# Performance work log

Hardware: AMD Instinct MI355X
Metric: run time of the kernel (lower is better)

Reference implementation:

```python
import jax, jax.numpy as jnp
import numpy as np

LN_EPS = 1e-5


def _layernorm(x, w, b):
    m = jnp.mean(x, axis=-1, keepdims=True)
    v = jnp.mean(jnp.square(x - m), axis=-1, keepdims=True)
    return (x - m) * jax.lax.rsqrt(v + LN_EPS) * w + b


def setup_inputs() -> dict:
    key = jax.random.key(0)
    k1, k2 = jax.random.split(key)
    B, S, D = 64, 512, 1024
    inputo = jax.random.normal(k1, (B, S, D), dtype=jnp.float32)
    W = jax.random.normal(k2, (2 * D, 4 * D), dtype=jnp.float32) * 0.02
    b = jnp.zeros((4 * D,), dtype=jnp.float32)
    ln_w = jnp.ones((4 * D,), dtype=jnp.float32)
    ln_b = jnp.zeros((4 * D,), dtype=jnp.float32)
    init_hx = jnp.zeros((1, D), dtype=jnp.float32)
    init_cx = jnp.zeros((1, D), dtype=jnp.float32)
    return {"inputo": inputo, "W": W, "b": b, "ln_w": ln_w, "ln_b": ln_b,
            "init_hx": init_hx, "init_cx": init_cx}


def reference(inputo, W, b, ln_w, ln_b, init_hx, init_cx):
    B, S, D = inputo.shape
    osize = init_hx.shape[1]
    hx = jnp.broadcast_to(init_hx, (B, osize))
    cx = jnp.broadcast_to(init_cx, (B, osize))

    def step(carry, x_t):
        h, c = carry
        comb = _layernorm(jnp.concatenate([x_t, h], axis=-1) @ W + b, ln_w, ln_b)
        comb = comb.reshape(B, 4, osize)
        gates = jax.nn.sigmoid(comb[:, :3])          # ig, fg, og
        hidden = jnp.tanh(comb[:, 3])
        c = gates[:, 1] * c + gates[:, 0] * hidden
        h = gates[:, 2] * jnp.tanh(c)
        return (h, c), h

    xs = jnp.swapaxes(inputo, 0, 1)                  # [S, B, D]
    _, outs = jax.lax.scan(step, (hx, cx), xs)       # [S, B, osize]
    return jnp.swapaxes(outs, 0, 1)                  # [B, S, osize]
```

## Files before the change

### kernel.cpp

```cpp
#include <hip/hip_runtime.h>
#include <hip/hip_bf16.h>


typedef __attribute__((ext_vector_type(8))) short bf16x8;
typedef __attribute__((ext_vector_type(16))) float f32x16;
typedef __attribute__((ext_vector_type(4)))  int   i32x4;

#define AT_RLX __ATOMIC_RELAXED
#define SC_AGT __HIP_MEMORY_SCOPE_AGENT


__global__ __launch_bounds__(256) void conv_w(const float* __restrict__ W,
                                              __hip_bfloat16* __restrict__ Wt) {
    size_t id = (size_t)blockIdx.x * 256 + threadIdx.x;
    int k = (int)(id >> 12);
    int n = (int)(id & 4095);
    Wt[(size_t)n * 2048 + k] = __float2bfloat16(W[id]);
}

__global__ __launch_bounds__(256) void conv_x(const float* __restrict__ X,
                                              __hip_bfloat16* __restrict__ Xt) {
    size_t id = (size_t)blockIdx.x * 256 + threadIdx.x;
    int d   = (int)(id & 1023);
    int row = (int)(id >> 10);
    int s = row >> 6;
    int b = row & 63;
    Xt[id] = __float2bfloat16(X[(((size_t)b * 512 + s) << 10) + d]);
}

__global__ __launch_bounds__(256) void init_misc(const float* __restrict__ hx,
                                                 __hip_bfloat16* __restrict__ h,
                                                 unsigned long long* __restrict__ comb2,
                                                 unsigned int* __restrict__ hflag) {
    int id = blockIdx.x * 256 + threadIdx.x;
    comb2[id] = 0ULL;
    if (id < 65536) h[id] = __float2bfloat16(hx[id & 1023]);
    if (id < 1024)  hflag[id] = 0u;
}

__device__ __forceinline__ i32x4 ld_cp16(const void* p) {
    i32x4 r;
    asm volatile("global_load_dwordx4 %0, %1, off sc0 sc1"
                 : "=&v"(r) : "v"(p) : "memory");
    return r;
}
__device__ __forceinline__ void vm_wait0() {
    asm volatile("s_waitcnt vmcnt(0)" ::: "memory");
    __builtin_amdgcn_sched_barrier(0);
}
__device__ __forceinline__ void xchg8u(unsigned long long* p, unsigned long long v) {
    unsigned long long old = __hip_atomic_exchange(p, v, AT_RLX, SC_AGT);
    asm volatile("" :: "v"(old));
}

__global__ __launch_bounds__(256, 1) void lstm_fused(
    const __hip_bfloat16* __restrict__ Xt,
    const __hip_bfloat16* __restrict__ Wt,
    __hip_bfloat16* __restrict__ h,
    const float* __restrict__ bias,
    const float* __restrict__ lnw,
    const float* __restrict__ lnb,
    const float* __restrict__ cx,
    unsigned long long* __restrict__ comb2,
    float* __restrict__ out,
    unsigned int* __restrict__ hflag)
{
    const int tid  = threadIdx.x;
    const int lane = tid & 63;
    const int wv   = tid >> 6;
    const int b    = blockIdx.x;

    const int nt = b >> 1;
    const int mt = b & 1;
    const int kc = wv;
    const int cl = lane & 31;
    const int hi = lane >> 5;
    const int kh = hi * 8;
    const int n0 = nt * 32;

    __shared__ float lds_f[8192];
    __shared__ short hstage[2][16384];
    __shared__ float red[8];

    const short* bp = (const short*)Wt + (size_t)(n0 + cl) * 2048 + kc * 512 + kh;
    bf16x8 breg[32];
#pragma unroll
    for (int i = 0; i < 32; ++i) breg[i] = *(const bf16x8*)(bp + i * 16);

    const short* xbase = (const short*)Xt + (size_t)(mt * 32 + cl) * 1024 + kc * 512 + kh;
    const short* hsrc = (const short*)h + (size_t)(mt * 32) * 1024 + (kc - 2) * 512 + lane * 8;
    const unsigned int* myhf = &hflag[(mt * 32 + cl) * 16];

    float cr[4];
    float bias_r[4][4], lnw_r[4][4], lnb_r[4][4];
    if (b < 64) {
#pragma unroll
        for (int e = 0; e < 4; ++e) cr[e] = cx[4 * tid + e];
#pragma unroll
        for (int g = 0; g < 4; ++g)
#pragma unroll
            for (int e = 0; e < 4; ++e) {
                bias_r[g][e] = bias[1024 * g + 4 * tid + e];
                lnw_r[g][e]  = lnw[1024 * g + 4 * tid + e];
                lnb_r[g][e]  = lnb[1024 * g + 4 * tid + e];
            }
    }

    for (int s = 0; s < 512; ++s) {
        f32x16 accA, accB;
#pragma unroll
        for (int i = 0; i < 16; ++i) { accA[i] = 0.f; accB[i] = 0.f; }
        if (kc < 2) {
            const short* ap = xbase + (size_t)s * 65536;
#pragma unroll
            for (int i = 0; i < 16; ++i) {
                bf16x8 a0 = *(const bf16x8*)(ap + i * 16);
                bf16x8 a1 = *(const bf16x8*)(ap + (i + 16) * 16);
                accA = __builtin_amdgcn_mfma_f32_32x32x16_bf16(a0, breg[i],      accA, 0, 0, 0);
                accB = __builtin_amdgcn_mfma_f32_32x32x16_bf16(a1, breg[i + 16], accB, 0, 0, 0);
            }
        } else {
            while (__hip_atomic_load(myhf, AT_RLX, SC_AGT) < (unsigned int)s)
                __builtin_amdgcn_s_sleep(1);
            asm volatile("" ::: "memory");
            i32x4 hb[32];
#pragma unroll
            for (int j = 0; j < 32; ++j)
                hb[j] = ld_cp16(hsrc + (size_t)j * 1024);
            vm_wait0();
            short* st = &hstage[kc - 2][0];
#pragma unroll
            for (int j = 0; j < 32; ++j)
                *(i32x4*)((char*)(st + j * 512) + ((lane * 16) ^ ((j & 7) << 4))) = hb[j];
            const char* rb = (const char*)(st + cl * 512);
            const int swz = (cl & 7) << 4;
#pragma unroll
            for (int i = 0; i < 16; ++i) {
                bf16x8 a0 = *(const bf16x8*)(rb + ((i * 32 + hi * 16) ^ swz));
                bf16x8 a1 = *(const bf16x8*)(rb + ((512 + i * 32 + hi * 16) ^ swz));
                accA = __builtin_amdgcn_mfma_f32_32x32x16_bf16(a0, breg[i],      accA, 0, 0, 0);
                accB = __builtin_amdgcn_mfma_f32_32x32x16_bf16(a1, breg[i + 16], accB, 0, 0, 0);
            }
        }
        float* lbuf = lds_f + (s & 1) * 4096;
#pragma unroll
        for (int r = 0; r < 16; ++r) {
            int rl = (r & 3) + 8 * (r >> 2) + 4 * (lane >> 5);
            lbuf[kc * 1024 + rl * 32 + cl] = accA[r] + accB[r];
        }
        __syncthreads();
        {
            unsigned long long ep64 = ((unsigned long long)(unsigned)(s + 1)) << 32;
#pragma unroll
            for (int half = 0; half < 2; ++half) {
                int e = 2 * tid + half * 512;
                float2 p0 = *(const float2*)&lbuf[e];
                float2 p1 = *(const float2*)&lbuf[1024 + e];
                float2 p2 = *(const float2*)&lbuf[2048 + e];
                float2 p3 = *(const float2*)&lbuf[3072 + e];
                float v0 = p0.x + p1.x + p2.x + p3.x;
                float v1 = p0.y + p1.y + p2.y + p3.y;
                size_t g = (size_t)(mt * 32 + (e >> 5)) * 4096 + n0 + (e & 31);
                __hip_atomic_store(&comb2[g],
                    ep64 | __builtin_bit_cast(unsigned int, v0), AT_RLX, SC_AGT);
                __hip_atomic_store(&comb2[g + 1],
                    ep64 | __builtin_bit_cast(unsigned int, v1), AT_RLX, SC_AGT);
            }
        }

        if (b < 64) {
            const unsigned long long* c2 = comb2 + (size_t)b * 4096;
            unsigned long long q[16];
            unsigned int miss = 0xFFFFu;
            const unsigned int tgt = (unsigned int)(s + 1);
            for (;;) {
#pragma unroll
                for (int g = 0; g < 4; ++g)
#pragma unroll
                    for (int e = 0; e < 4; ++e) {
                        int k = 4 * g + e;
                        if (miss & (1u << k))
                            q[k] = __hip_atomic_load(&c2[1024 * g + 4 * tid + e],
                                                     AT_RLX, SC_AGT);
                    }
                unsigned int nm = 0;
#pragma unroll
                for (int k = 0; k < 16; ++k)
                    if ((miss & (1u << k)) && (unsigned int)(q[k] >> 32) < tgt)
                        nm |= 1u << k;
                miss = nm;
                if (!miss) break;
                __builtin_amdgcn_s_sleep(1);
            }
            float v[4][4];
            float s1 = 0.f, s2 = 0.f;
#pragma unroll
            for (int g = 0; g < 4; ++g)
#pragma unroll
                for (int e = 0; e < 4; ++e) {
                    float x = __builtin_bit_cast(float, (unsigned int)q[4 * g + e])
                            + bias_r[g][e];
                    v[g][e] = x;
                    s1 += x;
                    s2 += x * x;
                }
            for (int off = 32; off; off >>= 1) {
                s1 += __shfl_down(s1, off);
                s2 += __shfl_down(s2, off);
            }
            if (lane == 0) { red[2 * wv] = s1; red[2 * wv + 1] = s2; }
            __syncthreads();
            float sum = red[0] + red[2] + red[4] + red[6];
            float ssq = red[1] + red[3] + red[5] + red[7];
            float mean = sum * (1.f / 4096.f);
            float var  = ssq * (1.f / 4096.f) - mean * mean;
            float rstd = rsqrtf(var + 1e-5f);
            float hn[4];
#pragma unroll
            for (int e = 0; e < 4; ++e) {
                float yi = (v[0][e] - mean) * rstd * lnw_r[0][e] + lnb_r[0][e];
                float yf = (v[1][e] - mean) * rstd * lnw_r[1][e] + lnb_r[1][e];
                float yo = (v[2][e] - mean) * rstd * lnw_r[2][e] + lnb_r[2][e];
                float yh = (v[3][e] - mean) * rstd * lnw_r[3][e] + lnb_r[3][e];
                float ig = 1.f / (1.f + __expf(-yi));
                float fg = 1.f / (1.f + __expf(-yf));
                float og = 1.f / (1.f + __expf(-yo));
                float hd = tanhf(yh);
                float cn = fg * cr[e] + ig * hd;
                cr[e] = cn;
                hn[e] = og * tanhf(cn);
            }
            unsigned long long hp = 0;
#pragma unroll
            for (int e = 0; e < 4; ++e)
                hp |= (unsigned long long)
                      __builtin_bit_cast(unsigned short, __float2bfloat16(hn[e])) << (16 * e);
            xchg8u((unsigned long long*)((unsigned short*)h + b * 1024 + 4 * tid), hp);
            __syncthreads();
            if (tid == 0)
                __hip_atomic_store(&hflag[b * 16], (unsigned int)(s + 1), AT_RLX, SC_AGT);
            float o4[4];
#pragma unroll
            for (int e = 0; e < 4; ++e) o4[e] = hn[e];
            *(float4*)(out + (size_t)b * 524288 + (size_t)s * 1024 + 4 * tid) =
                *(float4*)o4;
        }
    }
}

extern "C" void kernel_launch(void* const* d_in, const int* in_sizes, int n_in,
                              void* d_out, int out_size, void* d_ws, size_t ws_size,
                              hipStream_t stream) {
    const float* X   = (const float*)d_in[0];
    const float* W   = (const float*)d_in[1];
    const float* bv  = (const float*)d_in[2];
    const float* lnw = (const float*)d_in[3];
    const float* lnb = (const float*)d_in[4];
    const float* hx  = (const float*)d_in[5];
    const float* cx  = (const float*)d_in[6];
    float* out = (float*)d_out;

    char* base = (char*)d_ws;
    __hip_bfloat16*     Wt    = (__hip_bfloat16*)    (base);
    __hip_bfloat16*     Xt    = (__hip_bfloat16*)    (base + 16777216);
    unsigned long long* comb2 = (unsigned long long*)(base + 83886080);
    __hip_bfloat16*     hbuf  = (__hip_bfloat16*)    (base + 85983232);
    unsigned int*       hflag = (unsigned int*)      (base + 86114304);

    conv_w<<<32768, 256, 0, stream>>>(W, Wt);
    conv_x<<<131072, 256, 0, stream>>>(X, Xt);
    init_misc<<<1024, 256, 0, stream>>>(hx, hbuf, comb2, hflag);

    lstm_fused<<<256, 256, 0, stream>>>(Xt, Wt, hbuf, bv, lnw, lnb, cx, comb2, out,
                                        hflag);
}
```

Before: 5.061 ms.

## Embed epoch tags with h values to replace separate flag synchronization

The hidden-state buffer changes to 64-bit words that pair two bf16 h values with a step epoch. Consumers poll the data itself and retry only the loads whose epoch is stale, which removes the separate per-block flag, the extra __syncthreads and the flag store/poll round trip on each recurrent step. The cost is twice the bytes read and written for h, plus retry loops that can reissue global loads.

```diff
diff --git a/kernel.cpp b/kernel.cpp
--- a/kernel.cpp
+++ b/kernel.cpp
@@ -29,13 +29,16 @@
 }
 
 __global__ __launch_bounds__(256) void init_misc(const float* __restrict__ hx,
-                                                 __hip_bfloat16* __restrict__ h,
                                                  unsigned long long* __restrict__ comb2,
-                                                 unsigned int* __restrict__ hflag) {
+                                                 unsigned long long* __restrict__ hg) {
     int id = blockIdx.x * 256 + threadIdx.x;
     comb2[id] = 0ULL;
-    if (id < 65536) h[id] = __float2bfloat16(hx[id & 1023]);
-    if (id < 1024)  hflag[id] = 0u;
+    if (id < 32768) {
+        int col = (id & 511) * 2;
+        unsigned int lo = __builtin_bit_cast(unsigned short, __float2bfloat16(hx[col]));
+        unsigned int hi = __builtin_bit_cast(unsigned short, __float2bfloat16(hx[col + 1]));
+        hg[id] = (unsigned long long)(lo | (hi << 16));
+    }
 }
 
 __device__ __forceinline__ i32x4 ld_cp16(const void* p) {
@@ -48,22 +51,17 @@
     asm volatile("s_waitcnt vmcnt(0)" ::: "memory");
     __builtin_amdgcn_sched_barrier(0);
 }
-__device__ __forceinline__ void xchg8u(unsigned long long* p, unsigned long long v) {
-    unsigned long long old = __hip_atomic_exchange(p, v, AT_RLX, SC_AGT);
-    asm volatile("" :: "v"(old));
-}
 
 __global__ __launch_bounds__(256, 1) void lstm_fused(
     const __hip_bfloat16* __restrict__ Xt,
     const __hip_bfloat16* __restrict__ Wt,
-    __hip_bfloat16* __restrict__ h,
     const float* __restrict__ bias,
     const float* __restrict__ lnw,
     const float* __restrict__ lnb,
     const float* __restrict__ cx,
     unsigned long long* __restrict__ comb2,
-    float* __restrict__ out,
-    unsigned int* __restrict__ hflag)
+    unsigned long long* __restrict__ hg,
+    float* __restrict__ out)
 {
     const int tid  = threadIdx.x;
     const int lane = tid & 63;
@@ -88,8 +86,7 @@
     for (int i = 0; i < 32; ++i) breg[i] = *(const bf16x8*)(bp + i * 16);
 
     const short* xbase = (const short*)Xt + (size_t)(mt * 32 + cl) * 1024 + kc * 512 + kh;
-    const short* hsrc = (const short*)h + (size_t)(mt * 32) * 1024 + (kc - 2) * 512 + lane * 8;
-    const unsigned int* myhf = &hflag[(mt * 32 + cl) * 16];
+    const unsigned long long* hgw = hg + (size_t)(mt * 32) * 512 + (kc - 2) * 256;
 
     float cr[4];
     float bias_r[4][4], lnw_r[4][4], lnb_r[4][4];
@@ -120,19 +117,43 @@
                 accB = __builtin_amdgcn_mfma_f32_32x32x16_bf16(a1, breg[i + 16], accB, 0, 0, 0);
             }
         } else {
-            while (__hip_atomic_load(myhf, AT_RLX, SC_AGT) < (unsigned int)s)
-                __builtin_amdgcn_s_sleep(1);
-            asm volatile("" ::: "memory");
-            i32x4 hb[32];
-#pragma unroll
-            for (int j = 0; j < 32; ++j)
-                hb[j] = ld_cp16(hsrc + (size_t)j * 1024);
-            vm_wait0();
             short* st = &hstage[kc - 2][0];
 #pragma unroll
-            for (int j = 0; j < 32; ++j)
-                *(i32x4*)((char*)(st + j * 512) + ((lane * 16) ^ ((j & 7) << 4))) = hb[j];
-            const char* rb = (const char*)(st + cl * 512);
+            for (int bb = 0; bb < 4; ++bb) {
+                const int r0 = bb * 8;
+                i32x4 hb[16];
+                unsigned int mask = 0xFFFFu;
+                for (;;) {
+#pragma unroll
+                    for (int q = 0; q < 16; ++q)
+                        if (mask & (1u << q)) {
+                            int j = r0 + (q >> 1), p = q & 1;
+                            hb[q] = ld_cp16(hgw + (size_t)j * 512 + p * 128 + lane * 2);
+                        }
+                    vm_wait0();
+                    unsigned int nm = 0;
+#pragma unroll
+                    for (int q = 0; q < 16; ++q)
+                        if (mask & (1u << q)) {
+                            if ((unsigned int)hb[q][1] < (unsigned int)s ||
+                                (unsigned int)hb[q][3] < (unsigned int)s)
+                                nm |= 1u << q;
+                        }
+                    mask = nm;
+                    if (!mask) break;
+                    __builtin_amdgcn_s_sleep(1);
+                }
+#pragma unroll
+                for (int q = 0; q < 16; ++q) {
+                    int j = r0 + (q >> 1), p = q & 1;
+                    unsigned long long dv =
+                        (unsigned long long)(unsigned int)hb[q][0] |
+                        ((unsigned long long)(unsigned int)hb[q][2] << 32);
+                    *(unsigned long long*)((char*)st + j * 1024 +
+                        ((p * 512 + lane * 8) ^ ((j & 7) << 4))) = dv;
+                }
+            }
+            const char* rb = (const char*)st + cl * 1024;
             const int swz = (cl & 7) << 4;
 #pragma unroll
             for (int i = 0; i < 16; ++i) {
@@ -230,15 +251,15 @@
                 cr[e] = cn;
                 hn[e] = og * tanhf(cn);
             }
-            unsigned long long hp = 0;
-#pragma unroll
-            for (int e = 0; e < 4; ++e)
-                hp |= (unsigned long long)
-                      __builtin_bit_cast(unsigned short, __float2bfloat16(hn[e])) << (16 * e);
-            xchg8u((unsigned long long*)((unsigned short*)h + b * 1024 + 4 * tid), hp);
-            __syncthreads();
-            if (tid == 0)
-                __hip_atomic_store(&hflag[b * 16], (unsigned int)(s + 1), AT_RLX, SC_AGT);
+            unsigned short b0 = __builtin_bit_cast(unsigned short, __float2bfloat16(hn[0]));
+            unsigned short b1 = __builtin_bit_cast(unsigned short, __float2bfloat16(hn[1]));
+            unsigned short b2 = __builtin_bit_cast(unsigned short, __float2bfloat16(hn[2]));
+            unsigned short b3 = __builtin_bit_cast(unsigned short, __float2bfloat16(hn[3]));
+            unsigned long long ep64 = ((unsigned long long)(unsigned)(s + 1)) << 32;
+            __hip_atomic_store(&hg[(size_t)b * 512 + 2 * tid],
+                ep64 | (unsigned int)(b0 | ((unsigned int)b1 << 16)), AT_RLX, SC_AGT);
+            __hip_atomic_store(&hg[(size_t)b * 512 + 2 * tid + 1],
+                ep64 | (unsigned int)(b2 | ((unsigned int)b3 << 16)), AT_RLX, SC_AGT);
             float o4[4];
 #pragma unroll
             for (int e = 0; e < 4; ++e) o4[e] = hn[e];
@@ -264,13 +285,11 @@
     __hip_bfloat16*     Wt    = (__hip_bfloat16*)    (base);
     __hip_bfloat16*     Xt    = (__hip_bfloat16*)    (base + 16777216);
     unsigned long long* comb2 = (unsigned long long*)(base + 83886080);
-    __hip_bfloat16*     hbuf  = (__hip_bfloat16*)    (base + 85983232);
-    unsigned int*       hflag = (unsigned int*)      (base + 86114304);
+    unsigned long long* hg    = (unsigned long long*)(base + 85983232);
 
     conv_w<<<32768, 256, 0, stream>>>(W, Wt);
     conv_x<<<131072, 256, 0, stream>>>(X, Xt);
-    init_misc<<<1024, 256, 0, stream>>>(hx, hbuf, comb2, hflag);
-
-    lstm_fused<<<256, 256, 0, stream>>>(Xt, Wt, hbuf, bv, lnw, lnb, cx, comb2, out,
-                                        hflag);
-}
+    init_misc<<<1024, 256, 0, stream>>>(hx, comb2, hg);
+
+    lstm_fused<<<256, 256, 0, stream>>>(Xt, Wt, bv, lnw, lnb, cx, comb2, hg, out);
+}
```

Measured after the change: 7.540 ms. 49.0% more time.
